# Optimization experiments

Hardware: AMD Instinct MI355X
Metric: run time of the kernel (lower is better)

The kernel has to match this reference:

```python
import jax, jax.numpy as jnp
import numpy as np

B, P, D_MODEL = 16, 256, 1024
V, D_LLM = 1000, 4096
H, DK = 16, 64  # d_keys = d_model // n_heads


def setup_inputs() -> dict:
    key = jax.random.key(0)
    ks = jax.random.split(key, 11)
    s = lambda k, shape, fan: jax.random.normal(k, shape, jnp.float32) / np.sqrt(fan)
    return {
        "target_embedding": jax.random.normal(ks[0], (B, P, D_MODEL), jnp.float32),
        "source_embedding": jax.random.normal(ks[1], (V, D_LLM), jnp.float32),
        "value_embedding": jax.random.normal(ks[2], (V, D_LLM), jnp.float32),
        "Wq": s(ks[3], (D_MODEL, H * DK), D_MODEL),
        "bq": jnp.zeros((H * DK,), jnp.float32),
        "Wk": s(ks[4], (D_LLM, H * DK), D_LLM),
        "bk": jnp.zeros((H * DK,), jnp.float32),
        "Wv": s(ks[5], (D_LLM, H * DK), D_LLM),
        "bv": jnp.zeros((H * DK,), jnp.float32),
        "Wo": s(ks[6], (H * DK, D_LLM), H * DK),
        "bo": jnp.zeros((D_LLM,), jnp.float32),
    }


def reference(target_embedding, source_embedding, value_embedding,
              Wq, bq, Wk, bk, Wv, bv, Wo, bo):
    b, p, _ = target_embedding.shape
    v = source_embedding.shape[0]
    # projections
    Q = (target_embedding @ Wq + bq).reshape(b, p, H, DK)   # bphd
    K = (source_embedding @ Wk + bk).reshape(v, H, DK)      # vhd
    Vv = (value_embedding @ Wv + bv).reshape(v, H, DK)      # vhd
    scale = 1.0 / np.sqrt(DK)
    # NOTE: non-standard einsum — contracts over v, elementwise in d
    scores = jnp.einsum('bphd,vhd->bhpd', Q, K)             # [B,H,P,DK]
    A = jax.nn.softmax(scale * scores, axis=-1)             # softmax over head dim d
    # (dropout is identity in eval mode)
    R = jnp.einsum('bhpd,vhd->bphd', A, Vv)                 # A * sum_v V
    out = R.reshape(b, p, H * DK) @ Wo + bo                 # [B,P,D_LLM]
    return out
```

## Files before the change

kernel.cpp:

```cpp
#include <hip/hip_runtime.h>

#define BB   16
#define PP   256
#define BP   4096
#define DMODEL 1024
#define VV   1000
#define DLLM 4096
#define HH   16
#define DK   64
#define HDK  1024

using f32x4 = __attribute__((ext_vector_type(4))) float;
using s16x8 = __attribute__((ext_vector_type(8))) short;

__device__ __forceinline__ unsigned short f2bf(float f) {
    unsigned int u = __builtin_bit_cast(unsigned int, f);
    u = (u + 0x7FFFu + ((u >> 16) & 1u)) >> 16;
    return (unsigned short)u;
}

__device__ __forceinline__ void gload_lds16(const unsigned short* g, unsigned short* lds) {
    __builtin_amdgcn_global_load_lds(
        (const __attribute__((address_space(1))) void*)g,
        (__attribute__((address_space(3))) void*)lds,
        16, 0, 0);
}

__device__ __forceinline__ void transpose_body(const float* __restrict__ src,
                                               unsigned short* __restrict__ dst,
                                               int R, int C, int bx, int by, int t,
                                               float (*tile)[33]) {
    int tx = t & 31, ty = t >> 5;
    int c0 = bx * 32, r0 = by * 32;
#pragma unroll
    for (int j = 0; j < 4; ++j)
        tile[ty + j * 8][tx] = src[(size_t)(r0 + ty + j * 8) * C + c0 + tx];
    __syncthreads();
#pragma unroll
    for (int j = 0; j < 4; ++j)
        dst[(size_t)(c0 + ty + j * 8) * R + r0 + tx] = f2bf(tile[tx][ty + j * 8]);
}

__global__ void mega1(const float* __restrict__ src0, const float* __restrict__ src1,
                      float* __restrict__ part1,
                      const float* __restrict__ target, unsigned short* __restrict__ tgt_bf,
                      const float* __restrict__ Wq, unsigned short* __restrict__ wq_t,
                      const float* __restrict__ Wo, unsigned short* __restrict__ wo_t) {
    __shared__ float tile[32][33];
    int b = blockIdx.x, t = threadIdx.x;
    if (b < 1280) {
        int x = b & 15, y = (b >> 4) % 40, z = b / 640;
        int col = x * 256 + t;
        const float* src = z ? src1 : src0;
        int r0 = y * 25;
        float acc = 0.f;
        for (int r = 0; r < 25; ++r)
            acc += src[(size_t)(r0 + r) * DLLM + col];
        part1[((z * 40 + y) * DLLM) + col] = acc;
    } else if (b < 1280 + 4096) {
        int idx = (b - 1280) * 256 + t;
        float4 v = reinterpret_cast<const float4*>(target)[idx];
        ushort4 o = make_ushort4(f2bf(v.x), f2bf(v.y), f2bf(v.z), f2bf(v.w));
        reinterpret_cast<ushort4*>(tgt_bf)[idx] = o;
    } else if (b < 1280 + 4096 + 1024) {
        int b2 = b - 5376;
        transpose_body(Wq, wq_t, DMODEL, HDK, b2 & 31, b2 >> 5, t, tile);
    } else {
        int b2 = b - 6400;
        transpose_body(Wo, wo_t, HDK, DLLM, b2 & 127, b2 >> 7, t, tile);
    }
}

__global__ void gemv_partial2(const float* __restrict__ Wk, const float* __restrict__ Wv,
                              const float* __restrict__ part1, float* __restrict__ part2) {
    __shared__ float vec[64];
    int c     = blockIdx.x * 256 + threadIdx.x;
    int chunk = blockIdx.y;
    int z     = blockIdx.z;
    const float* W = z ? Wv : Wk;
    if (threadIdx.x < 64) {
        int r = chunk * 64 + threadIdx.x;
        float a = 0.f;
        for (int p = 0; p < 40; ++p)
            a += part1[(size_t)(z * 40 + p) * DLLM + r];
        vec[threadIdx.x] = a;
    }
    __syncthreads();
    float acc = 0.f;
    int r0 = chunk * 64;
    for (int r = 0; r < 64; ++r)
        acc += vec[r] * W[(size_t)(r0 + r) * HDK + c];
    part2[((z * 64 + chunk) * HDK) + c] = acc;
}

__global__ void gemv_reduce(const float* __restrict__ part,
                            const float* __restrict__ bk, const float* __restrict__ bv,
                            float* __restrict__ kvsum) {
    int idx = blockIdx.x * 256 + threadIdx.x;
    int z = idx >> 10, c = idx & 1023;
    float acc = 0.f;
    for (int ch = 0; ch < 64; ++ch) acc += part[(size_t)(z * 64 + ch) * HDK + c];
    acc += (float)VV * (z ? bv[c] : bk[c]);
    kvsum[idx] = acc;
}

#define BM 128
#define BN 128
#define BK2 32
#define LSTR 40

__global__ __launch_bounds__(256, 4)
void gemm_k(const unsigned short* __restrict__ A, const unsigned short* __restrict__ Bt,
            const float* __restrict__ bias,
            const float* __restrict__ kvsum, unsigned short* __restrict__ R,
            int M, int N, int K) {
    __shared__ unsigned short Asm[2][BM * LSTR];
    __shared__ unsigned short Bsm[2][BN * LSTR];
    const int t = threadIdx.x;
    const int wave = t >> 6, lane = t & 63;
    const int wr = wave >> 1, wc = wave & 1;
    const int bm = blockIdx.y * BM;
    const int bn = blockIdx.x * BN;
    const int l15 = lane & 15;
    const int kgrp = lane >> 4;

    const int srow = t >> 2, sc = (t & 3) * 8;
    const unsigned short* Ag0 = A + (size_t)(bm + srow) * K + sc;
    const unsigned short* Bg0 = Bt + (size_t)(bn + srow) * K + sc;
    const size_t rstep = (size_t)64 * K;
    const int off0 = srow * LSTR + sc, off1 = off0 + 64 * LSTR;

    f32x4 acc[4][4] = {};
    float4 ra0, ra1, rb0, rb1;

    ra0 = *reinterpret_cast<const float4*>(Ag0);
    ra1 = *reinterpret_cast<const float4*>(Ag0 + rstep);
    rb0 = *reinterpret_cast<const float4*>(Bg0);
    rb1 = *reinterpret_cast<const float4*>(Bg0 + rstep);
    *reinterpret_cast<float4*>(&Asm[0][off0]) = ra0;
    *reinterpret_cast<float4*>(&Asm[0][off1]) = ra1;
    *reinterpret_cast<float4*>(&Bsm[0][off0]) = rb0;
    *reinterpret_cast<float4*>(&Bsm[0][off1]) = rb1;

    const int nK = K / BK2;
    int cur = 0;
    for (int ks = 0; ks < nK; ++ks) {
        __syncthreads();
        if (ks + 1 < nK) {
            const unsigned short* Ap = Ag0 + (size_t)(ks + 1) * BK2;
            const unsigned short* Bp = Bg0 + (size_t)(ks + 1) * BK2;
            ra0 = *reinterpret_cast<const float4*>(Ap);
            ra1 = *reinterpret_cast<const float4*>(Ap + rstep);
            rb0 = *reinterpret_cast<const float4*>(Bp);
            rb1 = *reinterpret_cast<const float4*>(Bp + rstep);
        }
        s16x8 af[4], bfr[4];
#pragma unroll
        for (int m = 0; m < 4; ++m)
            af[m] = *reinterpret_cast<const s16x8*>(
                &Asm[cur][(wr * 64 + m * 16 + l15) * LSTR + kgrp * 8]);
#pragma unroll
        for (int n = 0; n < 4; ++n)
            bfr[n] = *reinterpret_cast<const s16x8*>(
                &Bsm[cur][(wc * 64 + n * 16 + l15) * LSTR + kgrp * 8]);
#pragma unroll
        for (int m = 0; m < 4; ++m)
#pragma unroll
            for (int n = 0; n < 4; ++n)
                acc[m][n] = __builtin_amdgcn_mfma_f32_16x16x32_bf16(af[m], bfr[n], acc[m][n], 0, 0, 0);
        if (ks + 1 < nK) {
            *reinterpret_cast<float4*>(&Asm[cur ^ 1][off0]) = ra0;
            *reinterpret_cast<float4*>(&Asm[cur ^ 1][off1]) = ra1;
            *reinterpret_cast<float4*>(&Bsm[cur ^ 1][off0]) = rb0;
            *reinterpret_cast<float4*>(&Bsm[cur ^ 1][off1]) = rb1;
        }
        cur ^= 1;
    }

    float bqv[4], ksv[4], vsv[4];
#pragma unroll
    for (int n = 0; n < 4; ++n) {
        int col = bn + wc * 64 + n * 16 + l15;
        bqv[n] = bias[col];
        ksv[n] = kvsum[col];
        vsv[n] = kvsum[HDK + col];
    }
#pragma unroll
    for (int m = 0; m < 4; ++m) {
        int grow = bm + wr * 64 + m * 16 + kgrp * 4;
#pragma unroll
        for (int j = 0; j < 4; ++j) {
            float x[4];
#pragma unroll
            for (int n = 0; n < 4; ++n)
                x[n] = 0.125f * (acc[m][n][j] + bqv[n]) * ksv[n];
            float mx = fmaxf(fmaxf(x[0], x[1]), fmaxf(x[2], x[3]));
#pragma unroll
            for (int off = 8; off; off >>= 1) mx = fmaxf(mx, __shfl_xor(mx, off));
            float e[4], s = 0.f;
#pragma unroll
            for (int n = 0; n < 4; ++n) { e[n] = __expf(x[n] - mx); s += e[n]; }
#pragma unroll
            for (int off = 8; off; off >>= 1) s += __shfl_xor(s, off);
            float inv = 1.0f / s;
#pragma unroll
            for (int n = 0; n < 4; ++n) {
                int col = bn + wc * 64 + n * 16 + l15;
                R[(size_t)(grow + j) * N + col] = f2bf(e[n] * inv * vsv[n]);
            }
        }
    }
}

#define G2_NT 32

__global__ __launch_bounds__(512, 2)
void gemm256(const unsigned short* __restrict__ A, const unsigned short* __restrict__ Bt,
             float* __restrict__ C, const float* __restrict__ bias, int N, int K) {
    __shared__ unsigned short Asm[4][8192];
    __shared__ unsigned short Bsm[4][8192];
    const int t = threadIdx.x;
    const int w = t >> 6, lane = t & 63;
    const int wr = w >> 2, wc = w & 3;
    const int l15 = lane & 15, kgrp = lane >> 4;
    const int bm = blockIdx.y * 256, bn = blockIdx.x * 256;

    size_t goffA[2], goffB[2];
    int ldsoff[2];
    {
        int s8 = lane & 7, jj = lane >> 3;
#pragma unroll
        for (int i = 0; i < 2; ++i) {
            int sr = i * 64 + w * 8 + jj;
            int x = s8 ^ (sr & 7);
            int row = sr * 2 + (x >> 2);
            int col = (x & 3) * 8;
            goffA[i] = (size_t)(bm + row) * K + col;
            goffB[i] = (size_t)(bn + row) * K + col;
            ldsoff[i] = i * 4096 + w * 512;
        }
    }
    int ra[8], rb[4];
#pragma unroll
    for (int m = 0; m < 8; ++m) {
        int r = wr * 128 + m * 16 + l15;
        int s8 = (kgrp + 4 * (r & 1)) ^ ((r >> 1) & 7);
        ra[m] = (r >> 1) * 64 + s8 * 8;
    }
#pragma unroll
    for (int n = 0; n < 4; ++n) {
        int r = wc * 64 + n * 16 + l15;
        int s8 = (kgrp + 4 * (r & 1)) ^ ((r >> 1) & 7);
        rb[n] = (r >> 1) * 64 + s8 * 8;
    }

    f32x4 acc[8][4] = {};

#define STAGE_A(tile_, buf_) do { size_t k0_ = (size_t)(tile_) * 32; \
    gload_lds16(A + goffA[0] + k0_, &Asm[buf_][ldsoff[0]]); \
    gload_lds16(A + goffA[1] + k0_, &Asm[buf_][ldsoff[1]]); } while (0)
#define STAGE_B(tile_, buf_) do { size_t k0_ = (size_t)(tile_) * 32; \
    gload_lds16(Bt + goffB[0] + k0_, &Bsm[buf_][ldsoff[0]]); \
    gload_lds16(Bt + goffB[1] + k0_, &Bsm[buf_][ldsoff[1]]); } while (0)

    STAGE_A(0, 0); STAGE_B(0, 0);
    STAGE_A(1, 1); STAGE_B(1, 1);
    asm volatile("s_waitcnt vmcnt(4)" ::: "memory");
    __builtin_amdgcn_s_barrier();

    for (int tk = 0; tk < G2_NT; ++tk) {
        const int buf = tk & 3;
        const unsigned short* As = Asm[buf];
        const unsigned short* Bs = Bsm[buf];
        s16x8 af[4], bfr[4];
#pragma unroll
        for (int m = 0; m < 4; ++m)
            af[m] = *reinterpret_cast<const s16x8*>(&As[ra[m]]);
#pragma unroll
        for (int n = 0; n < 4; ++n)
            bfr[n] = *reinterpret_cast<const s16x8*>(&Bs[rb[n]]);
        if (tk < G2_NT - 2) STAGE_A(tk + 2, (tk + 2) & 3);
        __builtin_amdgcn_s_barrier();
        __builtin_amdgcn_s_setprio(1);
#pragma unroll
        for (int m = 0; m < 4; ++m)
#pragma unroll
            for (int n = 0; n < 4; ++n)
                acc[m][n] = __builtin_amdgcn_mfma_f32_16x16x32_bf16(af[m], bfr[n], acc[m][n], 0, 0, 0);
        __builtin_amdgcn_s_setprio(0);
        __builtin_amdgcn_s_barrier();
        s16x8 af2[4];
#pragma unroll
        for (int m = 0; m < 4; ++m)
            af2[m] = *reinterpret_cast<const s16x8*>(&As[ra[m + 4]]);
        if (tk < G2_NT - 2) STAGE_B(tk + 2, (tk + 2) & 3);
        if (tk < G2_NT - 2)
            asm volatile("s_waitcnt vmcnt(4)" ::: "memory");
        else if (tk == G2_NT - 2)
            asm volatile("s_waitcnt vmcnt(0)" ::: "memory");
        __builtin_amdgcn_s_barrier();
        __builtin_amdgcn_s_setprio(1);
#pragma unroll
        for (int m = 0; m < 4; ++m)
#pragma unroll
            for (int n = 0; n < 4; ++n)
                acc[m + 4][n] = __builtin_amdgcn_mfma_f32_16x16x32_bf16(af2[m], bfr[n], acc[m + 4][n], 0, 0, 0);
        __builtin_amdgcn_s_setprio(0);
        __builtin_amdgcn_s_barrier();
    }
#undef STAGE_A
#undef STAGE_B

#pragma unroll
    for (int m = 0; m < 8; ++m) {
        int grow = bm + wr * 128 + m * 16 + kgrp * 4;
#pragma unroll
        for (int n = 0; n < 4; ++n) {
            int gcol = bn + wc * 64 + n * 16 + l15;
            float bb = bias[gcol];
#pragma unroll
            for (int j = 0; j < 4; ++j)
                C[(size_t)(grow + j) * N + gcol] = acc[m][n][j] + bb;
        }
    }
}

extern "C" void kernel_launch(void* const* d_in, const int* in_sizes, int n_in,
                              void* d_out, int out_size, void* d_ws, size_t ws_size,
                              hipStream_t stream) {
    const float* target = (const float*)d_in[0];
    const float* source = (const float*)d_in[1];
    const float* value  = (const float*)d_in[2];
    const float* Wq = (const float*)d_in[3];
    const float* bq = (const float*)d_in[4];
    const float* Wk = (const float*)d_in[5];
    const float* bk = (const float*)d_in[6];
    const float* Wv = (const float*)d_in[7];
    const float* bv = (const float*)d_in[8];
    const float* Wo = (const float*)d_in[9];
    const float* bo = (const float*)d_in[10];
    float* out = (float*)d_out;

    char* ws = (char*)d_ws;
    float*          part1  = (float*)(ws);
    float*          part2  = (float*)(ws + 0x180000);
    float*          kvsum  = (float*)(ws + 0x210000);
    unsigned short* tgt_bf = (unsigned short*)(ws + 0x400000);
    unsigned short* wq_t   = (unsigned short*)(ws + 0xC00000);
    unsigned short* wo_t   = (unsigned short*)(ws + 0xE00000);
    unsigned short* Rb     = (unsigned short*)(ws + 0x1600000);

    mega1<<<10496, 256, 0, stream>>>(source, value, part1, target, tgt_bf, Wq, wq_t, Wo, wo_t);

    gemv_partial2<<<dim3(4, 64, 2), 256, 0, stream>>>(Wk, Wv, part1, part2);
    gemv_reduce<<<8, 256, 0, stream>>>(part2, bk, bv, kvsum);

    gemm_k<<<dim3(HDK / BN, BP / BM), 256, 0, stream>>>(
        tgt_bf, wq_t, bq, kvsum, Rb, BP, HDK, DMODEL);

    gemm256<<<dim3(DLLM / 256, BP / 256), 512, 0, stream>>>(
        Rb, wo_t, out, bo, DLLM, HDK);
}
```

Measured before the change: 97.83 us.

## Unify both GEMMs into templated 4-stage direct-to-LDS pipelined kernel with XCD block remap

Replaces the register-staged double-buffered Q-projection GEMM and the 256x256 output GEMM with one templated kernel. The new kernel loads global memory straight into LDS, keeps three tiles in flight across four buffers, and uses one barrier per k-step instead of four. Work-group ids are remapped so consecutive tiles land on the same XCD, improving L2 reuse. The attention epilogue is kept as a template branch. The deeper prefetch and fewer barriers aim to hide memory latency, at the cost of more LDS use and less intra-iteration interleaving in the big GEMM.

```diff
diff --git a/kernel.cpp b/kernel.cpp
--- a/kernel.cpp
+++ b/kernel.cpp
@@ -104,146 +104,46 @@
     kvsum[idx] = acc;
 }
 
-#define BM 128
-#define BN 128
-#define BK2 32
-#define LSTR 40
-
-__global__ __launch_bounds__(256, 4)
-void gemm_k(const unsigned short* __restrict__ A, const unsigned short* __restrict__ Bt,
-            const float* __restrict__ bias,
-            const float* __restrict__ kvsum, unsigned short* __restrict__ R,
-            int M, int N, int K) {
-    __shared__ unsigned short Asm[2][BM * LSTR];
-    __shared__ unsigned short Bsm[2][BN * LSTR];
-    const int t = threadIdx.x;
-    const int wave = t >> 6, lane = t & 63;
-    const int wr = wave >> 1, wc = wave & 1;
-    const int bm = blockIdx.y * BM;
-    const int bn = blockIdx.x * BN;
-    const int l15 = lane & 15;
-    const int kgrp = lane >> 4;
-
-    const int srow = t >> 2, sc = (t & 3) * 8;
-    const unsigned short* Ag0 = A + (size_t)(bm + srow) * K + sc;
-    const unsigned short* Bg0 = Bt + (size_t)(bn + srow) * K + sc;
-    const size_t rstep = (size_t)64 * K;
-    const int off0 = srow * LSTR + sc, off1 = off0 + 64 * LSTR;
-
-    f32x4 acc[4][4] = {};
-    float4 ra0, ra1, rb0, rb1;
-
-    ra0 = *reinterpret_cast<const float4*>(Ag0);
-    ra1 = *reinterpret_cast<const float4*>(Ag0 + rstep);
-    rb0 = *reinterpret_cast<const float4*>(Bg0);
-    rb1 = *reinterpret_cast<const float4*>(Bg0 + rstep);
-    *reinterpret_cast<float4*>(&Asm[0][off0]) = ra0;
-    *reinterpret_cast<float4*>(&Asm[0][off1]) = ra1;
-    *reinterpret_cast<float4*>(&Bsm[0][off0]) = rb0;
-    *reinterpret_cast<float4*>(&Bsm[0][off1]) = rb1;
-
-    const int nK = K / BK2;
-    int cur = 0;
-    for (int ks = 0; ks < nK; ++ks) {
-        __syncthreads();
-        if (ks + 1 < nK) {
-            const unsigned short* Ap = Ag0 + (size_t)(ks + 1) * BK2;
-            const unsigned short* Bp = Bg0 + (size_t)(ks + 1) * BK2;
-            ra0 = *reinterpret_cast<const float4*>(Ap);
-            ra1 = *reinterpret_cast<const float4*>(Ap + rstep);
-            rb0 = *reinterpret_cast<const float4*>(Bp);
-            rb1 = *reinterpret_cast<const float4*>(Bp + rstep);
-        }
-        s16x8 af[4], bfr[4];
-#pragma unroll
-        for (int m = 0; m < 4; ++m)
-            af[m] = *reinterpret_cast<const s16x8*>(
-                &Asm[cur][(wr * 64 + m * 16 + l15) * LSTR + kgrp * 8]);
-#pragma unroll
-        for (int n = 0; n < 4; ++n)
-            bfr[n] = *reinterpret_cast<const s16x8*>(
-                &Bsm[cur][(wc * 64 + n * 16 + l15) * LSTR + kgrp * 8]);
-#pragma unroll
-        for (int m = 0; m < 4; ++m)
-#pragma unroll
-            for (int n = 0; n < 4; ++n)
-                acc[m][n] = __builtin_amdgcn_mfma_f32_16x16x32_bf16(af[m], bfr[n], acc[m][n], 0, 0, 0);
-        if (ks + 1 < nK) {
-            *reinterpret_cast<float4*>(&Asm[cur ^ 1][off0]) = ra0;
-            *reinterpret_cast<float4*>(&Asm[cur ^ 1][off1]) = ra1;
-            *reinterpret_cast<float4*>(&Bsm[cur ^ 1][off0]) = rb0;
-            *reinterpret_cast<float4*>(&Bsm[cur ^ 1][off1]) = rb1;
-        }
-        cur ^= 1;
-    }
-
-    float bqv[4], ksv[4], vsv[4];
-#pragma unroll
-    for (int n = 0; n < 4; ++n) {
-        int col = bn + wc * 64 + n * 16 + l15;
-        bqv[n] = bias[col];
-        ksv[n] = kvsum[col];
-        vsv[n] = kvsum[HDK + col];
-    }
-#pragma unroll
-    for (int m = 0; m < 4; ++m) {
-        int grow = bm + wr * 64 + m * 16 + kgrp * 4;
-#pragma unroll
-        for (int j = 0; j < 4; ++j) {
-            float x[4];
-#pragma unroll
-            for (int n = 0; n < 4; ++n)
-                x[n] = 0.125f * (acc[m][n][j] + bqv[n]) * ksv[n];
-            float mx = fmaxf(fmaxf(x[0], x[1]), fmaxf(x[2], x[3]));
-#pragma unroll
-            for (int off = 8; off; off >>= 1) mx = fmaxf(mx, __shfl_xor(mx, off));
-            float e[4], s = 0.f;
-#pragma unroll
-            for (int n = 0; n < 4; ++n) { e[n] = __expf(x[n] - mx); s += e[n]; }
-#pragma unroll
-            for (int off = 8; off; off >>= 1) s += __shfl_xor(s, off);
-            float inv = 1.0f / s;
-#pragma unroll
-            for (int n = 0; n < 4; ++n) {
-                int col = bn + wc * 64 + n * 16 + l15;
-                R[(size_t)(grow + j) * N + col] = f2bf(e[n] * inv * vsv[n]);
-            }
-        }
-    }
-}
-
-#define G2_NT 32
-
-__global__ __launch_bounds__(512, 2)
-void gemm256(const unsigned short* __restrict__ A, const unsigned short* __restrict__ Bt,
-             float* __restrict__ C, const float* __restrict__ bias, int N, int K) {
-    __shared__ unsigned short Asm[4][8192];
-    __shared__ unsigned short Bsm[4][8192];
+template<int EPI, int BMt, int BNt, int WM, int WN>
+__global__ __launch_bounds__(WM * WN * 64, 2)
+void gemm_ctd(const unsigned short* __restrict__ A, const unsigned short* __restrict__ Bt,
+              float* __restrict__ C, const float* __restrict__ bias,
+              const float* __restrict__ kvsum, unsigned short* __restrict__ R,
+              int N, int K, int gx) {
+    constexpr int WAVES = WM * WN;
+    constexpr int M_REP = BMt / WM / 16;
+    __shared__ unsigned short Asm[4][BMt * 32];
+    __shared__ unsigned short Bsm[4][BNt * 32];
+
+    const int nwg = gridDim.x, q = nwg >> 3;
+    const int nb = (blockIdx.x & 7) * q + (blockIdx.x >> 3);
+    const int bm = (nb / gx) * BMt;
+    const int bn = (nb % gx) * BNt;
+
     const int t = threadIdx.x;
     const int w = t >> 6, lane = t & 63;
-    const int wr = w >> 2, wc = w & 3;
+    const int wr = w / WN, wc = w % WN;
     const int l15 = lane & 15, kgrp = lane >> 4;
-    const int bm = blockIdx.y * 256, bn = blockIdx.x * 256;
 
     size_t goffA[2], goffB[2];
-    int ldsoff[2];
+    int ldso[2];
     {
         int s8 = lane & 7, jj = lane >> 3;
 #pragma unroll
         for (int i = 0; i < 2; ++i) {
-            int sr = i * 64 + w * 8 + jj;
+            int sr = (i * WAVES + w) * 8 + jj;
             int x = s8 ^ (sr & 7);
             int row = sr * 2 + (x >> 2);
             int col = (x & 3) * 8;
             goffA[i] = (size_t)(bm + row) * K + col;
             goffB[i] = (size_t)(bn + row) * K + col;
-            ldsoff[i] = i * 4096 + w * 512;
-        }
-    }
-    int ra[8], rb[4];
-#pragma unroll
-    for (int m = 0; m < 8; ++m) {
-        int r = wr * 128 + m * 16 + l15;
+            ldso[i] = (i * WAVES + w) * 512;
+        }
+    }
+    int ra[M_REP], rb[4];
+#pragma unroll
+    for (int m = 0; m < M_REP; ++m) {
+        int r = wr * (M_REP * 16) + m * 16 + l15;
         int s8 = (kgrp + 4 * (r & 1)) ^ ((r >> 1) & 7);
         ra[m] = (r >> 1) * 64 + s8 * 8;
     }
@@ -254,73 +154,89 @@
         rb[n] = (r >> 1) * 64 + s8 * 8;
     }
 
-    f32x4 acc[8][4] = {};
-
-#define STAGE_A(tile_, buf_) do { size_t k0_ = (size_t)(tile_) * 32; \
-    gload_lds16(A + goffA[0] + k0_, &Asm[buf_][ldsoff[0]]); \
-    gload_lds16(A + goffA[1] + k0_, &Asm[buf_][ldsoff[1]]); } while (0)
-#define STAGE_B(tile_, buf_) do { size_t k0_ = (size_t)(tile_) * 32; \
-    gload_lds16(Bt + goffB[0] + k0_, &Bsm[buf_][ldsoff[0]]); \
-    gload_lds16(Bt + goffB[1] + k0_, &Bsm[buf_][ldsoff[1]]); } while (0)
-
-    STAGE_A(0, 0); STAGE_B(0, 0);
-    STAGE_A(1, 1); STAGE_B(1, 1);
-    asm volatile("s_waitcnt vmcnt(4)" ::: "memory");
+    f32x4 acc[M_REP][4] = {};
+
+#define STAGE(t_, b_) do { size_t k0_ = (size_t)(t_) * 32;            \
+    gload_lds16(A + goffA[0] + k0_, &Asm[b_][ldso[0]]);               \
+    gload_lds16(A + goffA[1] + k0_, &Asm[b_][ldso[1]]);               \
+    gload_lds16(Bt + goffB[0] + k0_, &Bsm[b_][ldso[0]]);              \
+    gload_lds16(Bt + goffB[1] + k0_, &Bsm[b_][ldso[1]]); } while (0)
+
+    const int nT = K >> 5;
+    STAGE(0, 0); STAGE(1, 1); STAGE(2, 2);
+    asm volatile("s_waitcnt vmcnt(8)" ::: "memory");
     __builtin_amdgcn_s_barrier();
 
-    for (int tk = 0; tk < G2_NT; ++tk) {
-        const int buf = tk & 3;
-        const unsigned short* As = Asm[buf];
-        const unsigned short* Bs = Bsm[buf];
-        s16x8 af[4], bfr[4];
-#pragma unroll
-        for (int m = 0; m < 4; ++m)
-            af[m] = *reinterpret_cast<const s16x8*>(&As[ra[m]]);
+    for (int tk = 0; tk < nT; ++tk) {
+        const int b = tk & 3;
+        s16x8 af[M_REP], bfr[4];
+#pragma unroll
+        for (int m = 0; m < M_REP; ++m)
+            af[m] = *reinterpret_cast<const s16x8*>(&Asm[b][ra[m]]);
 #pragma unroll
         for (int n = 0; n < 4; ++n)
-            bfr[n] = *reinterpret_cast<const s16x8*>(&Bs[rb[n]]);
-        if (tk < G2_NT - 2) STAGE_A(tk + 2, (tk + 2) & 3);
-        __builtin_amdgcn_s_barrier();
+            bfr[n] = *reinterpret_cast<const s16x8*>(&Bsm[b][rb[n]]);
+        if (tk < nT - 3) STAGE(tk + 3, (tk + 3) & 3);
         __builtin_amdgcn_s_setprio(1);
 #pragma unroll
-        for (int m = 0; m < 4; ++m)
+        for (int m = 0; m < M_REP; ++m)
 #pragma unroll
             for (int n = 0; n < 4; ++n)
                 acc[m][n] = __builtin_amdgcn_mfma_f32_16x16x32_bf16(af[m], bfr[n], acc[m][n], 0, 0, 0);
         __builtin_amdgcn_s_setprio(0);
-        __builtin_amdgcn_s_barrier();
-        s16x8 af2[4];
-#pragma unroll
-        for (int m = 0; m < 4; ++m)
-            af2[m] = *reinterpret_cast<const s16x8*>(&As[ra[m + 4]]);
-        if (tk < G2_NT - 2) STAGE_B(tk + 2, (tk + 2) & 3);
-        if (tk < G2_NT - 2)
-            asm volatile("s_waitcnt vmcnt(4)" ::: "memory");
-        else if (tk == G2_NT - 2)
-            asm volatile("s_waitcnt vmcnt(0)" ::: "memory");
-        __builtin_amdgcn_s_barrier();
-        __builtin_amdgcn_s_setprio(1);
-#pragma unroll
-        for (int m = 0; m < 4; ++m)
-#pragma unroll
-            for (int n = 0; n < 4; ++n)
-                acc[m + 4][n] = __builtin_amdgcn_mfma_f32_16x16x32_bf16(af2[m], bfr[n], acc[m + 4][n], 0, 0, 0);
-        __builtin_amdgcn_s_setprio(0);
-        __builtin_amdgcn_s_barrier();
-    }
-#undef STAGE_A
-#undef STAGE_B
-
-#pragma unroll
-    for (int m = 0; m < 8; ++m) {
-        int grow = bm + wr * 128 + m * 16 + kgrp * 4;
+        if (tk < nT - 3)       asm volatile("s_waitcnt vmcnt(8)" ::: "memory");
+        else if (tk == nT - 3) asm volatile("s_waitcnt vmcnt(4)" ::: "memory");
+        else if (tk == nT - 2) asm volatile("s_waitcnt vmcnt(0)" ::: "memory");
+        if (tk + 1 < nT) __builtin_amdgcn_s_barrier();
+    }
+#undef STAGE
+
+    if (EPI == 0) {
+#pragma unroll
+        for (int m = 0; m < M_REP; ++m) {
+            int grow = bm + wr * (M_REP * 16) + m * 16 + kgrp * 4;
+#pragma unroll
+            for (int n = 0; n < 4; ++n) {
+                int gcol = bn + wc * 64 + n * 16 + l15;
+                float bb = bias[gcol];
+#pragma unroll
+                for (int j = 0; j < 4; ++j)
+                    C[(size_t)(grow + j) * N + gcol] = acc[m][n][j] + bb;
+            }
+        }
+    } else {
+        float bqv[4], ksv[4], vsv[4];
 #pragma unroll
         for (int n = 0; n < 4; ++n) {
-            int gcol = bn + wc * 64 + n * 16 + l15;
-            float bb = bias[gcol];
-#pragma unroll
-            for (int j = 0; j < 4; ++j)
-                C[(size_t)(grow + j) * N + gcol] = acc[m][n][j] + bb;
+            int col = bn + wc * 64 + n * 16 + l15;
+            bqv[n] = bias[col];
+            ksv[n] = kvsum[col];
+            vsv[n] = kvsum[HDK + col];
+        }
+#pragma unroll
+        for (int m = 0; m < M_REP; ++m) {
+            int grow = bm + wr * (M_REP * 16) + m * 16 + kgrp * 4;
+#pragma unroll
+            for (int j = 0; j < 4; ++j) {
+                float x[4];
+#pragma unroll
+                for (int n = 0; n < 4; ++n)
+                    x[n] = 0.125f * (acc[m][n][j] + bqv[n]) * ksv[n];
+                float mx = fmaxf(fmaxf(x[0], x[1]), fmaxf(x[2], x[3]));
+#pragma unroll
+                for (int off = 8; off; off >>= 1) mx = fmaxf(mx, __shfl_xor(mx, off));
+                float e[4], s = 0.f;
+#pragma unroll
+                for (int n = 0; n < 4; ++n) { e[n] = __expf(x[n] - mx); s += e[n]; }
+#pragma unroll
+                for (int off = 8; off; off >>= 1) s += __shfl_xor(s, off);
+                float inv = 1.0f / s;
+#pragma unroll
+                for (int n = 0; n < 4; ++n) {
+                    int col = bn + wc * 64 + n * 16 + l15;
+                    R[(size_t)(grow + j) * N + col] = f2bf(e[n] * inv * vsv[n]);
+                }
+            }
         }
     }
 }
@@ -355,9 +271,9 @@
     gemv_partial2<<<dim3(4, 64, 2), 256, 0, stream>>>(Wk, Wv, part1, part2);
     gemv_reduce<<<8, 256, 0, stream>>>(part2, bk, bv, kvsum);
 
-    gemm_k<<<dim3(HDK / BN, BP / BM), 256, 0, stream>>>(
-        tgt_bf, wq_t, bq, kvsum, Rb, BP, HDK, DMODEL);
-
-    gemm256<<<dim3(DLLM / 256, BP / 256), 512, 0, stream>>>(
-        Rb, wo_t, out, bo, DLLM, HDK);
-}
+    gemm_ctd<1, 128, 128, 2, 2><<<256, 256, 0, stream>>>(
+        tgt_bf, wq_t, nullptr, bq, kvsum, Rb, HDK, DMODEL, HDK / 128);
+
+    gemm_ctd<0, 256, 256, 2, 4><<<256, 512, 0, stream>>>(
+        Rb, wo_t, out, bo, nullptr, nullptr, DLLM, HDK, DLLM / 256);
+}
```

After: 95.27 us. 1.03x faster.
